# Kernel optimization log

Hardware: AMD Instinct MI355X
Metric: run time of the kernel (lower is better)

The kernel has to match this reference:

```python
import jax, jax.numpy as jnp
import numpy as np

B, N, T = 1, 1024, 2048   # batch, graph nodes, timesteps
E, K = 16384, 32          # edges, causal kernel taps


def setup_inputs() -> dict:
    key = jax.random.key(0)
    k1, k2, k3, k4 = jax.random.split(key, 4)
    x = jax.random.normal(k1, (B, N, T), dtype=jnp.float32)
    # per-edge causal impulse-response kernels (aggregator(g) output)
    kernel = jax.random.normal(k2, (E, K), dtype=jnp.float32) * 0.1
    src = jax.random.randint(k3, (E,), 0, N)
    dst = jax.random.randint(k4, (E,), 0, N)
    return {"x": x, "kernel": kernel, "src": src, "dst": dst}


def reference(x, kernel, src, dst):
    # Block-sparse causal conv over the edge list:
    #   y_e[b, t] = sum_k kernel[e, k] * x[b, src_e, t - k]   (causal)
    #   out[b, n, t] = x[b, n, t] + sum_{e: dst_e = n} y_e[b, t]
    # (residual applied because g.include_index_diag is False)
    xs = x[:, src, :]                      # [B, E, T] gather upstream signals
    rhs = kernel[:, None, ::-1]            # [E, 1, K] flipped -> true causal conv
    y = jax.lax.conv_general_dilated(
        xs, rhs,
        window_strides=(1,),
        padding=[(K - 1, 0)],              # left-pad: strictly causal
        dimension_numbers=("NCW", "OIW", "NCW"),
        feature_group_count=E,             # one independent kernel per edge
    )                                      # [B, E, T]
    agg = jax.ops.segment_sum(jnp.swapaxes(y, 0, 1), dst, num_segments=N)  # [N, B, T]
    return x + jnp.swapaxes(agg, 0, 1)     # [B, N, T]
```

## Files before the change

kernel.cpp:

```cpp
#include <hip/hip_runtime.h>
#include <hip/hip_bf16.h>

#define TT  2048
#define KK  32
#define NN  1024
#define EE  16384
#define CAP 64
#define RS  2080

typedef short short8  __attribute__((ext_vector_type(8)));
typedef short short4v __attribute__((ext_vector_type(4)));
typedef float f32x4   __attribute__((ext_vector_type(4)));

__device__ short g_xbf[NN * RS];
__device__ short g_kbf[EE * KK];

__device__ __forceinline__ short f2bf(float f) {
    __hip_bfloat16 h = __float2bfloat16(f);
    return __builtin_bit_cast(short, h);
}

__global__ __launch_bounds__(256) void cvt_kernel(const float* __restrict__ x,
                                                  const float* __restrict__ kern,
                                                  int* __restrict__ cnt) {
    const int bid = blockIdx.x, tid = threadIdx.x;
    if (bid < NN) {
        const float4* xr = (const float4*)(x + (size_t)bid * TT);
        const float4 u = xr[2 * tid], v = xr[2 * tid + 1];
        short8 h;
        h[0]=f2bf(u.x); h[1]=f2bf(u.y); h[2]=f2bf(u.z); h[3]=f2bf(u.w);
        h[4]=f2bf(v.x); h[5]=f2bf(v.y); h[6]=f2bf(v.z); h[7]=f2bf(v.w);
        *(short8*)&g_xbf[(size_t)bid * RS + 32 + 8 * tid] = h;
        if (tid < 4) {
            short8 z; z[0]=0;z[1]=0;z[2]=0;z[3]=0;z[4]=0;z[5]=0;z[6]=0;z[7]=0;
            *(short8*)&g_xbf[(size_t)bid * RS + 8 * tid] = z;
        }
    } else if (bid == NN) {
        ((int4*)cnt)[tid] = make_int4(0, 0, 0, 0);
    } else {
        const int i = (bid - NN - 1) * 256 + tid;
        const float4* k4 = (const float4*)kern;
        const float4 u = k4[2 * i], v = k4[2 * i + 1];
        short8 h;
        h[0]=f2bf(u.x); h[1]=f2bf(u.y); h[2]=f2bf(u.z); h[3]=f2bf(u.w);
        h[4]=f2bf(v.x); h[5]=f2bf(v.y); h[6]=f2bf(v.z); h[7]=f2bf(v.w);
        ((short8*)g_kbf)[i] = h;
    }
}

__global__ __launch_bounds__(256) void csr_kernel(const int* __restrict__ src,
                                                  const int* __restrict__ dst,
                                                  int* __restrict__ cnt,
                                                  unsigned* __restrict__ slots) {
    const int e = blockIdx.x * 256 + threadIdx.x;
    const int d = dst[e];
    const int p = atomicAdd(&cnt[d], 1);
    if (p < CAP) slots[(size_t)d * CAP + p] = ((unsigned)src[e] << 14) | (unsigned)e;
}

__global__ __launch_bounds__(128, 6) void lti_kernel(
    const float*    __restrict__ x,
    const int*      __restrict__ cnt,
    const unsigned* __restrict__ slots,
    float*          __restrict__ out)
{
    const int bid = blockIdx.x;
    const int n   = bid >> 2;
    const int w   = bid & 3;
    const int tid = threadIdx.x;
    const int pw  = tid >> 6;
    const int ln  = tid & 63;
    const int c   = ln & 15, g = ln >> 4;
    const int t0  = 512 * w;
    const int D   = 16 * c + 8 * g;

    __shared__ __align__(16) short kt_all[2][8][72];
    __shared__ __align__(16) float red[512];
    __shared__ unsigned bl[CAP];

    short (*kt)[72] = kt_all[pw];

    short8 z8; z8[0]=0;z8[1]=0;z8[2]=0;z8[3]=0;z8[4]=0;z8[5]=0;z8[6]=0;z8[7]=0;

    {
        short8* kz = (short8*)&kt[0][0];
        kz[ln] = z8;
        if (ln < 8) kz[64 + ln] = z8;
    }
    if (tid < CAP) bl[tid] = slots[(size_t)n * CAP + tid];
    int L = cnt[n]; if (L > CAP) L = CAP;
    __syncthreads();

    const int M = (L - pw + 1) >> 1;
    #define IDX(I) (pw + 2 * (I))

    f32x4 acc0 = {0,0,0,0}, acc1 = {0,0,0,0};
    short8  xa0A, xb0A, xa1A, xb1A, xa0B, xb0B, xa1B, xb1B;
    short4v trA, trB;

    const int a_ = c & 7;
    const int s1 = ((a_ + 1) & 7) + 15 - c + 8 * g;

    #define LOADV(S, P)                                                                \
    {                                                                                  \
        const unsigned sv = bl[P];                                                     \
        const int e0 = __builtin_amdgcn_readfirstlane((int)(sv & 16383u));             \
        const int s0 = __builtin_amdgcn_readfirstlane((int)(sv >> 14));                \
        const short* rb = g_xbf + (size_t)s0 * RS + t0 + D;                            \
        xa0##S = *(const short8*)(rb);                                                 \
        xb0##S = *(const short8*)(rb + 16);                                            \
        xa1##S = *(const short8*)(rb + 256);                                           \
        xb1##S = *(const short8*)(rb + 272);                                           \
        tr##S  = *(const short4v*)(g_kbf + ((size_t)e0 << 5) + 4 * (ln & 7));          \
    }

    #define COMMIT(S)                                                                  \
    {                                                                                  \
        const int a2 = ln >> 3, pad = (a2 + 1) & 7, mb = 4 * (ln & 7);                 \
        kt[a2][pad + 47 - mb] = tr##S[0];                                              \
        kt[a2][pad + 46 - mb] = tr##S[1];                                              \
        kt[a2][pad + 45 - mb] = tr##S[2];                                              \
        kt[a2][pad + 44 - mb] = tr##S[3];                                              \
    }

    #define COMPUTE(S)                                                                 \
    {                                                                                  \
        const short8 b1 = *(const short8*)&kt[a_][s1];                                 \
        short8 b2 = *(const short8*)&kt[a_][s1 + 16];                                  \
        if (g < 2) b2 = z8;                              \
        acc0 = __builtin_amdgcn_mfma_f32_16x16x32_bf16(xa0##S, b1, acc0, 0, 0, 0);     \
        acc0 = __builtin_amdgcn_mfma_f32_16x16x32_bf16(xb0##S, b2, acc0, 0, 0, 0);     \
        acc1 = __builtin_amdgcn_mfma_f32_16x16x32_bf16(xa1##S, b1, acc1, 0, 0, 0);     \
        acc1 = __builtin_amdgcn_mfma_f32_16x16x32_bf16(xb1##S, b2, acc1, 0, 0, 0);     \
    }

    if (M > 0) {
        LOADV(A, IDX(0));
        if (M > 1) LOADV(B, IDX(1));
        for (int i = 0; i < M; i += 2) {
            COMMIT(A);
            COMPUTE(A);
            if (i + 2 < M) LOADV(A, IDX(i + 2));
            if (i + 1 < M) { COMMIT(B); COMPUTE(B); }
            if (i + 3 < M) LOADV(B, IDX(i + 3));
        }
    }

    if (pw == 1) {
        #pragma unroll
        for (int qd = 0; qd < 4; ++qd) {
            const int ta = 64 * g + 16 * qd + c;
            red[ta]       = acc0[qd];
            red[256 + ta] = acc1[qd];
        }
    }
    __syncthreads();
    if (pw == 0) {
        const float* xr  = x   + (size_t)n * TT + t0;
        float*       orw = out + (size_t)n * TT + t0;
        #pragma unroll
        for (int qd = 0; qd < 4; ++qd) {
            const int ta = 64 * g + 16 * qd + c;
            orw[ta]       = xr[ta]       + acc0[qd] + red[ta];
            orw[256 + ta] = xr[256 + ta] + acc1[qd] + red[256 + ta];
        }
    }
    #undef IDX
    #undef LOADV
    #undef COMMIT
    #undef COMPUTE
}

extern "C" void kernel_launch(void* const* d_in, const int* in_sizes, int n_in,
                              void* d_out, int out_size, void* d_ws, size_t ws_size,
                              hipStream_t stream) {
    const float* x    = (const float*)d_in[0];
    const float* kern = (const float*)d_in[1];
    const int*   src  = (const int*)d_in[2];
    const int*   dst  = (const int*)d_in[3];
    float*       out  = (float*)d_out;

    int*      cnt   = (int*)d_ws;
    unsigned* slots = (unsigned*)((char*)d_ws + 4096);

    cvt_kernel<<<dim3(NN + 1 + EE * KK / 8 / 256), dim3(256), 0, stream>>>(x, kern, cnt);
    csr_kernel<<<dim3(EE / 256), dim3(256), 0, stream>>>(src, dst, cnt, slots);
    lti_kernel<<<dim3(NN * 4), dim3(128), 0, stream>>>(x, cnt, slots, out);
}
```

Baseline: 35.87 us.

## Prebuild reversed zero-padded kernel layout in global memory, drop LDS staging

The conversion kernel now writes each edge's kernel as a 256-element bf16 block holding reversed, zero-padded copies at two parities. The conv kernel can then load its MFMA B operands straight from global memory instead of scattering taps into shared memory and reading them back. The main loop is also deepened to a three-stage register prefetch, and the occupancy hint drops from 6 to 4 to make room for the extra registers. The cost is an 8x larger kernel buffer and extra conversion blocks, plus more global load traffic per edge.

```diff
diff --git a/kernel.cpp b/kernel.cpp
--- a/kernel.cpp
+++ b/kernel.cpp
@@ -9,11 +9,10 @@
 #define RS  2080
 
 typedef short short8  __attribute__((ext_vector_type(8)));
-typedef short short4v __attribute__((ext_vector_type(4)));
 typedef float f32x4   __attribute__((ext_vector_type(4)));
 
 __device__ short g_xbf[NN * RS];
-__device__ short g_kbf[EE * KK];
+__device__ short g_krev[EE * 256];
 
 __device__ __forceinline__ short f2bf(float f) {
     __hip_bfloat16 h = __float2bfloat16(f);
@@ -38,13 +37,17 @@
     } else if (bid == NN) {
         ((int4*)cnt)[tid] = make_int4(0, 0, 0, 0);
     } else {
-        const int i = (bid - NN - 1) * 256 + tid;
-        const float4* k4 = (const float4*)kern;
-        const float4 u = k4[2 * i], v = k4[2 * i + 1];
-        short8 h;
-        h[0]=f2bf(u.x); h[1]=f2bf(u.y); h[2]=f2bf(u.z); h[3]=f2bf(u.w);
-        h[4]=f2bf(v.x); h[5]=f2bf(v.y); h[6]=f2bf(v.z); h[7]=f2bf(v.w);
-        ((short8*)g_kbf)[i] = h;
+        const int v = tid >> 6, j = tid & 63;
+        const int e = (bid - NN - 1) * 4 + v;
+        const float* kp = kern + (size_t)e * KK;
+        short v0 = 0, v1 = 0;
+        if (j >= 16 && j < 48) v0 = f2bf(kp[47 - j]);
+        if (j >= 15 && j < 47) v1 = f2bf(kp[46 - j]);
+        short* kb = g_krev + ((size_t)e << 8);
+        kb[j]       = v0;
+        kb[64 + j]  = 0;
+        kb[128 + j] = v1;
+        kb[192 + j] = 0;
     }
 }
 
@@ -58,7 +61,7 @@
     if (p < CAP) slots[(size_t)d * CAP + p] = ((unsigned)src[e] << 14) | (unsigned)e;
 }
 
-__global__ __launch_bounds__(128, 6) void lti_kernel(
+__global__ __launch_bounds__(128, 4) void lti_kernel(
     const float*    __restrict__ x,
     const int*      __restrict__ cnt,
     const unsigned* __restrict__ slots,
@@ -74,19 +77,9 @@
     const int t0  = 512 * w;
     const int D   = 16 * c + 8 * g;
 
-    __shared__ __align__(16) short kt_all[2][8][72];
     __shared__ __align__(16) float red[512];
     __shared__ unsigned bl[CAP];
 
-    short (*kt)[72] = kt_all[pw];
-
-    short8 z8; z8[0]=0;z8[1]=0;z8[2]=0;z8[3]=0;z8[4]=0;z8[5]=0;z8[6]=0;z8[7]=0;
-
-    {
-        short8* kz = (short8*)&kt[0][0];
-        kz[ln] = z8;
-        if (ln < 8) kz[64 + ln] = z8;
-    }
     if (tid < CAP) bl[tid] = slots[(size_t)n * CAP + tid];
     int L = cnt[n]; if (L > CAP) L = CAP;
     __syncthreads();
@@ -94,12 +87,16 @@
     const int M = (L - pw + 1) >> 1;
     #define IDX(I) (pw + 2 * (I))
 
+    const int idx   = 15 - c + 8 * g;
+    const int par   = idx & 1;
+    const int koff1 = idx - par;
+    const int koff2 = (g < 2) ? 96 : koff1 + 16;
+    const int kvar  = par << 7;
+
     f32x4 acc0 = {0,0,0,0}, acc1 = {0,0,0,0};
-    short8  xa0A, xb0A, xa1A, xb1A, xa0B, xb0B, xa1B, xb1B;
-    short4v trA, trB;
-
-    const int a_ = c & 7;
-    const int s1 = ((a_ + 1) & 7) + 15 - c + 8 * g;
+    short8 xa0A, xb0A, xa1A, xb1A, kb1A, kb2A;
+    short8 xa0B, xb0B, xa1B, xb1B, kb1B, kb2B;
+    short8 xa0C, xb0C, xa1C, xb1C, kb1C, kb2C;
 
     #define LOADV(S, P)                                                                \
     {                                                                                  \
@@ -111,38 +108,34 @@
         xb0##S = *(const short8*)(rb + 16);                                            \
         xa1##S = *(const short8*)(rb + 256);                                           \
         xb1##S = *(const short8*)(rb + 272);                                           \
-        tr##S  = *(const short4v*)(g_kbf + ((size_t)e0 << 5) + 4 * (ln & 7));          \
-    }
-
-    #define COMMIT(S)                                                                  \
-    {                                                                                  \
-        const int a2 = ln >> 3, pad = (a2 + 1) & 7, mb = 4 * (ln & 7);                 \
-        kt[a2][pad + 47 - mb] = tr##S[0];                                              \
-        kt[a2][pad + 46 - mb] = tr##S[1];                                              \
-        kt[a2][pad + 45 - mb] = tr##S[2];                                              \
-        kt[a2][pad + 44 - mb] = tr##S[3];                                              \
+        const short* kb = g_krev + ((size_t)e0 << 8) + kvar;                           \
+        kb1##S = *(const short8*)(kb + koff1);                                         \
+        kb2##S = *(const short8*)(kb + koff2);                                         \
     }
 
     #define COMPUTE(S)                                                                 \
     {                                                                                  \
-        const short8 b1 = *(const short8*)&kt[a_][s1];                                 \
-        short8 b2 = *(const short8*)&kt[a_][s1 + 16];                                  \
-        if (g < 2) b2 = z8;                              \
-        acc0 = __builtin_amdgcn_mfma_f32_16x16x32_bf16(xa0##S, b1, acc0, 0, 0, 0);     \
-        acc0 = __builtin_amdgcn_mfma_f32_16x16x32_bf16(xb0##S, b2, acc0, 0, 0, 0);     \
-        acc1 = __builtin_amdgcn_mfma_f32_16x16x32_bf16(xa1##S, b1, acc1, 0, 0, 0);     \
-        acc1 = __builtin_amdgcn_mfma_f32_16x16x32_bf16(xb1##S, b2, acc1, 0, 0, 0);     \
+        acc0 = __builtin_amdgcn_mfma_f32_16x16x32_bf16(xa0##S, kb1##S, acc0, 0, 0, 0); \
+        acc0 = __builtin_amdgcn_mfma_f32_16x16x32_bf16(xb0##S, kb2##S, acc0, 0, 0, 0); \
+        acc1 = __builtin_amdgcn_mfma_f32_16x16x32_bf16(xa1##S, kb1##S, acc1, 0, 0, 0); \
+        acc1 = __builtin_amdgcn_mfma_f32_16x16x32_bf16(xb1##S, kb2##S, acc1, 0, 0, 0); \
     }
 
     if (M > 0) {
         LOADV(A, IDX(0));
         if (M > 1) LOADV(B, IDX(1));
-        for (int i = 0; i < M; i += 2) {
-            COMMIT(A);
+        if (M > 2) LOADV(C, IDX(2));
+        for (int i = 0; i < M; i += 3) {
             COMPUTE(A);
-            if (i + 2 < M) LOADV(A, IDX(i + 2));
-            if (i + 1 < M) { COMMIT(B); COMPUTE(B); }
-            if (i + 3 < M) LOADV(B, IDX(i + 3));
+            if (i + 3 < M) LOADV(A, IDX(i + 3));
+            if (i + 1 < M) {
+                COMPUTE(B);
+                if (i + 4 < M) LOADV(B, IDX(i + 4));
+            }
+            if (i + 2 < M) {
+                COMPUTE(C);
+                if (i + 5 < M) LOADV(C, IDX(i + 5));
+            }
         }
     }
 
@@ -167,7 +160,6 @@
     }
     #undef IDX
     #undef LOADV
-    #undef COMMIT
     #undef COMPUTE
 }
 
@@ -183,7 +175,7 @@
     int*      cnt   = (int*)d_ws;
     unsigned* slots = (unsigned*)((char*)d_ws + 4096);
 
-    cvt_kernel<<<dim3(NN + 1 + EE * KK / 8 / 256), dim3(256), 0, stream>>>(x, kern, cnt);
+    cvt_kernel<<<dim3(NN + 1 + EE / 4), dim3(256), 0, stream>>>(x, kern, cnt);
     csr_kernel<<<dim3(EE / 256), dim3(256), 0, stream>>>(src, dst, cnt, slots);
     lti_kernel<<<dim3(NN * 4), dim3(128), 0, stream>>>(x, cnt, slots, out);
 }
```

After: 39.44 us. 1.1x slower.

## Process full rows per block with async global-to-LDS triple-buffered source loads

Applied to the files above, without the earlier changes.

Each block now handles one destination node across all 2048 timesteps instead of a quarter, so every source row is read once per node. The row is streamed into LDS with global_load_lds in a three-stage buffer, with explicit vmcnt waits. Kernel taps are converted from fp32 to bf16 inside the main kernel, which drops the separate kernel-conversion pass. The trade-offs are a grid four times smaller (1024 blocks), a much larger LDS footprint, 32 accumulator registers per lane, and hand-counted waitcnts that depend on how the compiler orders instructions.

```diff
diff --git a/kernel.cpp b/kernel.cpp
--- a/kernel.cpp
+++ b/kernel.cpp
@@ -8,20 +8,23 @@
 #define CAP 64
 #define RS  2080
 
-typedef short short8  __attribute__((ext_vector_type(8)));
-typedef short short4v __attribute__((ext_vector_type(4)));
-typedef float f32x4   __attribute__((ext_vector_type(4)));
+typedef short short8 __attribute__((ext_vector_type(8)));
+typedef float f32x4  __attribute__((ext_vector_type(4)));
 
 __device__ short g_xbf[NN * RS];
-__device__ short g_kbf[EE * KK];
 
 __device__ __forceinline__ short f2bf(float f) {
     __hip_bfloat16 h = __float2bfloat16(f);
     return __builtin_bit_cast(short, h);
 }
 
+__device__ __forceinline__ void gload_lds16(const short* g, short* l) {
+    __builtin_amdgcn_global_load_lds(
+        (const __attribute__((address_space(1))) void*)(const void*)(g),
+        (__attribute__((address_space(3))) void*)(void*)(l), 16, 0, 0);
+}
+
 __global__ __launch_bounds__(256) void cvt_kernel(const float* __restrict__ x,
-                                                  const float* __restrict__ kern,
                                                   int* __restrict__ cnt) {
     const int bid = blockIdx.x, tid = threadIdx.x;
     if (bid < NN) {
@@ -35,16 +38,8 @@
             short8 z; z[0]=0;z[1]=0;z[2]=0;z[3]=0;z[4]=0;z[5]=0;z[6]=0;z[7]=0;
             *(short8*)&g_xbf[(size_t)bid * RS + 8 * tid] = z;
         }
-    } else if (bid == NN) {
+    } else {
         ((int4*)cnt)[tid] = make_int4(0, 0, 0, 0);
-    } else {
-        const int i = (bid - NN - 1) * 256 + tid;
-        const float4* k4 = (const float4*)kern;
-        const float4 u = k4[2 * i], v = k4[2 * i + 1];
-        short8 h;
-        h[0]=f2bf(u.x); h[1]=f2bf(u.y); h[2]=f2bf(u.z); h[3]=f2bf(u.w);
-        h[4]=f2bf(v.x); h[5]=f2bf(v.y); h[6]=f2bf(v.z); h[7]=f2bf(v.w);
-        ((short8*)g_kbf)[i] = h;
     }
 }
 
@@ -58,27 +53,27 @@
     if (p < CAP) slots[(size_t)d * CAP + p] = ((unsigned)src[e] << 14) | (unsigned)e;
 }
 
-__global__ __launch_bounds__(128, 6) void lti_kernel(
+__global__ __launch_bounds__(128, 2) void lti_kernel(
     const float*    __restrict__ x,
+    const float*    __restrict__ kern,
     const int*      __restrict__ cnt,
     const unsigned* __restrict__ slots,
     float*          __restrict__ out)
 {
-    const int bid = blockIdx.x;
-    const int n   = bid >> 2;
-    const int w   = bid & 3;
+    const int n   = blockIdx.x;
     const int tid = threadIdx.x;
     const int pw  = tid >> 6;
     const int ln  = tid & 63;
     const int c   = ln & 15, g = ln >> 4;
-    const int t0  = 512 * w;
     const int D   = 16 * c + 8 * g;
 
+    __shared__ __align__(16) short xs_all[2][3][RS];
     __shared__ __align__(16) short kt_all[2][8][72];
-    __shared__ __align__(16) float red[512];
+    __shared__ __align__(16) float red[TT];
     __shared__ unsigned bl[CAP];
 
-    short (*kt)[72] = kt_all[pw];
+    short (*xsb)[RS] = xs_all[pw];
+    short (*kt)[72]  = kt_all[pw];
 
     short8 z8; z8[0]=0;z8[1]=0;z8[2]=0;z8[3]=0;z8[4]=0;z8[5]=0;z8[6]=0;z8[7]=0;
 
@@ -94,33 +89,36 @@
     const int M = (L - pw + 1) >> 1;
     #define IDX(I) (pw + 2 * (I))
 
-    f32x4 acc0 = {0,0,0,0}, acc1 = {0,0,0,0};
-    short8  xa0A, xb0A, xa1A, xb1A, xa0B, xb0B, xa1B, xb1B;
-    short4v trA, trB;
+    f32x4 acc[8];
+    #pragma unroll
+    for (int s = 0; s < 8; ++s) { acc[s][0]=0.f; acc[s][1]=0.f; acc[s][2]=0.f; acc[s][3]=0.f; }
+
+    float4 tr0, tr1, tr2;
 
     const int a_ = c & 7;
     const int s1 = ((a_ + 1) & 7) + 15 - c + 8 * g;
 
-    #define LOADV(S, P)                                                                \
+    #define ISSUE(S, P)                                                                \
     {                                                                                  \
         const unsigned sv = bl[P];                                                     \
         const int e0 = __builtin_amdgcn_readfirstlane((int)(sv & 16383u));             \
         const int s0 = __builtin_amdgcn_readfirstlane((int)(sv >> 14));                \
-        const short* rb = g_xbf + (size_t)s0 * RS + t0 + D;                            \
-        xa0##S = *(const short8*)(rb);                                                 \
-        xb0##S = *(const short8*)(rb + 16);                                            \
-        xa1##S = *(const short8*)(rb + 256);                                           \
-        xb1##S = *(const short8*)(rb + 272);                                           \
-        tr##S  = *(const short4v*)(g_kbf + ((size_t)e0 << 5) + 4 * (ln & 7));          \
+        const short* rb = g_xbf + (size_t)s0 * RS;                                     \
+        gload_lds16(rb + 8 * ln,        &xsb[S][0]);                                   \
+        gload_lds16(rb + 8 * ln + 512,  &xsb[S][512]);                                 \
+        gload_lds16(rb + 8 * ln + 1024, &xsb[S][1024]);                                \
+        gload_lds16(rb + 8 * ln + 1536, &xsb[S][1536]);                                \
+        if (ln < 4) gload_lds16(rb + 8 * ln + 2048, &xsb[S][2048]);                    \
+        tr##S = *(const float4*)(kern + ((size_t)e0 << 5) + 4 * (ln & 7));             \
     }
 
     #define COMMIT(S)                                                                  \
     {                                                                                  \
         const int a2 = ln >> 3, pad = (a2 + 1) & 7, mb = 4 * (ln & 7);                 \
-        kt[a2][pad + 47 - mb] = tr##S[0];                                              \
-        kt[a2][pad + 46 - mb] = tr##S[1];                                              \
-        kt[a2][pad + 45 - mb] = tr##S[2];                                              \
-        kt[a2][pad + 44 - mb] = tr##S[3];                                              \
+        kt[a2][pad + 47 - mb] = f2bf(tr##S.x);                                         \
+        kt[a2][pad + 46 - mb] = f2bf(tr##S.y);                                         \
+        kt[a2][pad + 45 - mb] = f2bf(tr##S.z);                                         \
+        kt[a2][pad + 44 - mb] = f2bf(tr##S.w);                                         \
     }
 
     #define COMPUTE(S)                                                                 \
@@ -128,47 +126,61 @@
         const short8 b1 = *(const short8*)&kt[a_][s1];                                 \
         short8 b2 = *(const short8*)&kt[a_][s1 + 16];                                  \
         if (g < 2) b2 = z8;                              \
-        acc0 = __builtin_amdgcn_mfma_f32_16x16x32_bf16(xa0##S, b1, acc0, 0, 0, 0);     \
-        acc0 = __builtin_amdgcn_mfma_f32_16x16x32_bf16(xb0##S, b2, acc0, 0, 0, 0);     \
-        acc1 = __builtin_amdgcn_mfma_f32_16x16x32_bf16(xa1##S, b1, acc1, 0, 0, 0);     \
-        acc1 = __builtin_amdgcn_mfma_f32_16x16x32_bf16(xb1##S, b2, acc1, 0, 0, 0);     \
-    }
-
-    if (M > 0) {
-        LOADV(A, IDX(0));
-        if (M > 1) LOADV(B, IDX(1));
-        for (int i = 0; i < M; i += 2) {
-            COMMIT(A);
-            COMPUTE(A);
-            if (i + 2 < M) LOADV(A, IDX(i + 2));
-            if (i + 1 < M) { COMMIT(B); COMPUTE(B); }
-            if (i + 3 < M) LOADV(B, IDX(i + 3));
-        }
+        _Pragma("unroll")                                                              \
+        for (int s = 0; s < 8; ++s) {                                                  \
+            const short8 a1  = *(const short8*)&xsb[S][256 * s + D];                   \
+            const short8 a2v = *(const short8*)&xsb[S][256 * s + D + 16];              \
+            acc[s] = __builtin_amdgcn_mfma_f32_16x16x32_bf16(a1,  b1, acc[s], 0,0,0);  \
+            acc[s] = __builtin_amdgcn_mfma_f32_16x16x32_bf16(a2v, b2, acc[s], 0,0,0);  \
+        }                                                                              \
+    }
+
+    #define BODY(SC, SN, I)                                                            \
+    if ((I) < M) {                                                                     \
+        __builtin_amdgcn_sched_barrier(0);                                             \
+        if ((I) + 2 < M) ISSUE(SN, IDX((I) + 2));                                      \
+        const int rem = M - (I);                                                       \
+        if (rem >= 3)      { asm volatile("s_waitcnt vmcnt(12)" ::: "memory"); }       \
+        else if (rem == 2) { asm volatile("s_waitcnt vmcnt(6)"  ::: "memory"); }       \
+        else               { asm volatile("s_waitcnt vmcnt(0)"  ::: "memory"); }       \
+        __builtin_amdgcn_sched_barrier(0);                                             \
+        COMMIT(SC);                                                                    \
+        COMPUTE(SC);                                                                   \
+    }
+
+    if (M > 0) ISSUE(0, IDX(0));
+    if (M > 1) ISSUE(1, IDX(1));
+    for (int i = 0; i < M; i += 3) {
+        BODY(0, 2, i);
+        BODY(1, 0, i + 1);
+        BODY(2, 1, i + 2);
     }
 
     if (pw == 1) {
         #pragma unroll
-        for (int qd = 0; qd < 4; ++qd) {
-            const int ta = 64 * g + 16 * qd + c;
-            red[ta]       = acc0[qd];
-            red[256 + ta] = acc1[qd];
-        }
+        for (int s = 0; s < 8; ++s)
+            #pragma unroll
+            for (int qd = 0; qd < 4; ++qd)
+                red[256 * s + 64 * g + 16 * qd + c] = acc[s][qd];
     }
     __syncthreads();
     if (pw == 0) {
-        const float* xr  = x   + (size_t)n * TT + t0;
-        float*       orw = out + (size_t)n * TT + t0;
+        const float* xr  = x   + (size_t)n * TT;
+        float*       orw = out + (size_t)n * TT;
         #pragma unroll
-        for (int qd = 0; qd < 4; ++qd) {
-            const int ta = 64 * g + 16 * qd + c;
-            orw[ta]       = xr[ta]       + acc0[qd] + red[ta];
-            orw[256 + ta] = xr[256 + ta] + acc1[qd] + red[256 + ta];
+        for (int s = 0; s < 8; ++s) {
+            #pragma unroll
+            for (int qd = 0; qd < 4; ++qd) {
+                const int ta = 256 * s + 64 * g + 16 * qd + c;
+                orw[ta] = xr[ta] + acc[s][qd] + red[ta];
+            }
         }
     }
     #undef IDX
-    #undef LOADV
+    #undef ISSUE
     #undef COMMIT
     #undef COMPUTE
+    #undef BODY
 }
 
 extern "C" void kernel_launch(void* const* d_in, const int* in_sizes, int n_in,
@@ -183,7 +195,7 @@
     int*      cnt   = (int*)d_ws;
     unsigned* slots = (unsigned*)((char*)d_ws + 4096);
 
-    cvt_kernel<<<dim3(NN + 1 + EE * KK / 8 / 256), dim3(256), 0, stream>>>(x, kern, cnt);
+    cvt_kernel<<<dim3(NN + 1), dim3(256), 0, stream>>>(x, cnt);
     csr_kernel<<<dim3(EE / 256), dim3(256), 0, stream>>>(src, dst, cnt, slots);
-    lti_kernel<<<dim3(NN * 4), dim3(128), 0, stream>>>(x, cnt, slots, out);
-}
+    lti_kernel<<<dim3(NN), dim3(128), 0, stream>>>(x, kern, cnt, slots, out);
+}
```

Measured after the change: 34.72 us (median of 2 runs). 3.2% less time.
